# Kernel tuning notes

Measured on AMD Instinct MI355X. Metric: run time of the kernel, lower is better.

## Reference

```python
import jax, jax.numpy as jnp
import numpy as np

NEG = -9e15
ALPHA = 0.2  # leakyrelu slope


def setup_inputs() -> dict:
    key = jax.random.key(0)
    ks = jax.random.split(key, 12)
    bs, N, Fx, F, D = 8, 512, 8, 64, 16
    return {
        'input': jax.random.normal(ks[0], (bs, N, 1), jnp.float32),
        'adj': jax.random.randint(ks[1], (N, N), 0, 2, jnp.int32),
        'ext_input': jax.random.normal(ks[2], (bs, N, Fx), jnp.float32),
        'side_input': jax.random.normal(ks[3], (bs, N, 1), jnp.float32),
        'W': jax.random.normal(ks[4], (1, F), jnp.float32),
        'a': jax.random.normal(ks[5], (2 * F, 1), jnp.float32),
        'WS': jax.random.normal(ks[6], (1, F), jnp.float32),
        'aS': jax.random.normal(ks[7], (2 * F, 1), jnp.float32),
        'WQ': jax.random.normal(ks[8], (2, D), jnp.float32),
        'WK': jax.random.normal(ks[9], (2, D), jnp.float32),
        'WV': jax.random.normal(ks[10], (1, F), jnp.float32),
    }


def _pair_scores(h, a_vec):
    # e[b,i,j] = leakyrelu(a . [h_i, h_j]) ; equivalent to h@a1 + (h@a2)^T
    F = h.shape[-1]
    s1 = h @ a_vec[:F]          # [b,N,1]
    s2 = h @ a_vec[F:]          # [b,N,1]
    return jax.nn.leaky_relu(s1 + jnp.swapaxes(s2, 1, 2), negative_slope=ALPHA)


def reference(input, adj, ext_input, side_input, W, a, WS, aS, WQ, WK, WV):
    bs, N, _ = input.shape
    Fx = ext_input.shape[-1]
    D = WQ.shape[1]
    mask = (adj > 0)[None, :, :]  # [1,N,N] broadcasts over batch

    # ---- Step 1: node-channel GAT attention ----
    h = input @ W                    # [b,N,F]
    e = _pair_scores(h, a)           # [b,N,N]
    att = jnp.where(mask, e, NEG)
    h_side = side_input @ WS         # [b,N,F]
    e_side = _pair_scores(h_side, aS)
    att_side = jnp.where(mask, e_side, NEG)
    att = att + att_side
    att = jnp.where(att > 0, att, NEG)
    att = jax.nn.softmax(att, axis=2)             # [b,N,N]
    h_prime = jnp.einsum('bij,bjf->bif', att, h)  # [b,N,F]

    # ---- Step 2: ext-feature dot-product attention ----
    xs = input[..., 0]  # [b,N]
    # q[b,i,j,d] = (x_i*WQ[0,d] + x_j*WQ[1,d]) / sqrt(D)
    q = (xs[:, :, None, None] * WQ[0] + xs[:, None, :, None] * WQ[1]) / (D ** 0.5)
    # k[b,i,j,d,f] = ext_i_f*WK[0,d] + ext_j_f*WK[1,d]; dot = sum_d q*k, computed fused:
    qk0 = q @ WK[0]   # [b,N,N]
    qk1 = q @ WK[1]   # [b,N,N]
    dot = ext_input[:, :, None, :] * qk0[..., None] + ext_input[:, None, :, :] * qk1[..., None]  # [b,N,N,Fx]
    dot = jnp.where(dot > 0, dot, NEG)
    dot = jax.nn.softmax(dot, axis=3)
    final = dot * att[..., None]                 # [b,N,N,Fx]
    v = ext_input[..., None] * WV[0][None, None, None, :]  # [b,N,Fx,F]
    ext_rep = jnp.einsum('bijf,bife->bie', final, v)       # sum over j and f -> [b,N,F]

    return jax.nn.elu(h_prime), jax.nn.elu(ext_rep)
```

## Files before the change

kernel.cpp:

```cpp
#include <hip/hip_runtime.h>

#define NEGV (-9e15f)
#define LOG2E 1.44269504088896340736f

template<int CTRL>
__device__ __forceinline__ float dpp_add(float v) {
    const int t = __builtin_amdgcn_update_dpp(0, __float_as_int(v), CTRL, 0xf, 0xf, false);
    return v + __int_as_float(t);
}
template<int CTRL>
__device__ __forceinline__ float dpp_fmax(float v) {
    const int t = __builtin_amdgcn_update_dpp(__float_as_int(v), __float_as_int(v),
                                              CTRL, 0xf, 0xf, false);
    return fmaxf(v, __int_as_float(t));
}
__device__ __forceinline__ float rdlane(float v, int l) {
    return __int_as_float(__builtin_amdgcn_readlane(__float_as_int(v), l));
}
__device__ __forceinline__ float wsum(float v) {
    v = dpp_add<0x111>(v);
    v = dpp_add<0x112>(v);
    v = dpp_add<0x114>(v);
    v = dpp_add<0x118>(v);
    v = dpp_add<0x142>(v);
    v = dpp_add<0x143>(v);
    return rdlane(v, 63);
}
__device__ __forceinline__ float wmax(float v) {
    v = dpp_fmax<0x111>(v);
    v = dpp_fmax<0x112>(v);
    v = dpp_fmax<0x114>(v);
    v = dpp_fmax<0x118>(v);
    v = dpp_fmax<0x142>(v);
    v = dpp_fmax<0x143>(v);
    return rdlane(v, 63);
}
__device__ __forceinline__ float rowscan16(float v) {
    v = dpp_add<0x111>(v);
    v = dpp_add<0x112>(v);
    v = dpp_add<0x114>(v);
    v = dpp_add<0x118>(v);
    return v;
}
__device__ __forceinline__ void ld8f(const float* p, float* o) {
    const float4 v0 = ((const float4*)p)[0];
    const float4 v1 = ((const float4*)p)[1];
    o[0] = v0.x; o[1] = v0.y; o[2] = v0.z; o[3] = v0.w;
    o[4] = v1.x; o[5] = v1.y; o[6] = v1.z; o[7] = v1.w;
}

__global__ __launch_bounds__(64) void sentinel_kernel(float* __restrict__ out) {
    out[blockIdx.x * 64 + threadIdx.x] = 111222.0f;
}

__global__ __launch_bounds__(128, 4) void gat_fused_f32(
    const float* __restrict__ input, const int* __restrict__ adj,
    const float* __restrict__ ext, const float* __restrict__ side,
    const float* __restrict__ W, const float* __restrict__ a,
    const float* __restrict__ WS, const float* __restrict__ aS,
    const float* __restrict__ WQ, const float* __restrict__ WK,
    const float* __restrict__ WV, float* __restrict__ out)
{
    const int N = 512, F = 64;
    const int lane = threadIdx.x & 63;
    const int w = threadIdx.x >> 6;
    const int b = blockIdx.x >> 8;
    const int i0 = (blockIdx.x & 255) * 2;

    __shared__ float mrg[16];

    const int jbase = 256 * w;

    const float* ebase = ext + (size_t)(b * N + jbase) * 8;
    float4 stA[4], stB[4];
#pragma unroll
    for (int u = 0; u < 4; u++) {
        const float* p = ebase + (size_t)(u * 64 + lane) * 8;
        stA[u] = ((const float4*)p)[0];
        stB[u] = ((const float4*)p)[1];
    }

    const bool adj64 = (__any(adj[2 * lane + 1] != 0) == 0);

    const float wf  = W[lane];
    const float wvf = WV[lane];
    const float c1  = wsum(wf * a[lane]) * LOG2E;
    const float c2  = wsum(wf * a[F + lane]) * LOG2E;
    const float wsf = WS[lane];
    const float cS1 = wsum(wsf * aS[lane]) * LOG2E;
    const float cS2 = wsum(wsf * aS[F + lane]) * LOG2E;

    const int g = lane >> 4, l16 = lane & 15;
    const float QS = 0.25f * LOG2E;
    float prod = WQ[(g >> 1) * 16 + l16] * WK[(g & 1) * 16 + l16];
    prod = rowscan16(prod);
    const float a00 = rdlane(prod, 15) * QS;
    const float a01 = rdlane(prod, 31) * QS;
    const float a10 = rdlane(prod, 47) * QS;
    const float a11 = rdlane(prod, 63) * QS;

    const int row0 = b * N + i0;
    const float x0 = input[row0], x1 = input[row0 + 1];
    const float y0 = side[row0],  y1 = side[row0 + 1];
    float ei0[8], ei1[8];
    ld8f(ext + (size_t)row0 * 8, ei0);
    ld8f(ext + (size_t)(row0 + 1) * 8, ei1);

    const float s10 = c1 * x0,  s11 = c1 * x1;
    const float t10 = cS1 * y0, t11 = cS1 * y1;

    const float* xp = input + b * N + jbase;
    const float* yp = side + b * N + jbase;
    const int arow0 = i0 * N + jbase;
    const int* adji0 = adj + arow0;
    const int* adji1 = adji0 + N;
    const long long* adjl0 = (const long long*)adj + arow0;
    const long long* adjl1 = adjl0 + N;

    float xj[4], L0[4], L1[4];
#pragma unroll
    for (int t = 0; t < 4; t++) {
        const int jj = lane + 64 * t;
        const float xv = xp[jj];
        const float yv = yp[jj];
        xj[t] = xv;
        const float z  = c2 * xv;
        const float zs = cS2 * yv;
        float u0 = s10 + z;  u0 = fmaxf(u0, 0.2f * u0);
        float v0 = t10 + zs; v0 = fmaxf(v0, 0.2f * v0);
        float u1 = s11 + z;  u1 = fmaxf(u1, 0.2f * u1);
        float v1 = t11 + zs; v1 = fmaxf(v1, 0.2f * v1);
        const float g0 = u0 + v0;
        const float g1 = u1 + v1;
        int m0, m1;
        if (adj64) { m0 = (adjl0[jj] != 0); m1 = (adjl1[jj] != 0); }
        else       { m0 = adji0[jj];        m1 = adji1[jj]; }
        L0[t] = (m0 != 0 && g0 > 0.f) ? g0 : NEGV;
        L1[t] = (m1 != 0 && g1 > 0.f) ? g1 : NEGV;
    }
    float M0 = fmaxf(fmaxf(L0[0], L0[1]), fmaxf(L0[2], L0[3]));
    float M1 = fmaxf(fmaxf(L1[0], L1[1]), fmaxf(L1[2], L1[3]));
    M0 = wmax(M0); M1 = wmax(M1);

    float s0 = 0.f, s1 = 0.f;
#pragma unroll
    for (int t = 0; t < 4; t++) {
        L0[t] = __builtin_amdgcn_exp2f(L0[t] - M0); s0 += L0[t];
        L1[t] = __builtin_amdgcn_exp2f(L1[t] - M1); s1 += L1[t];
    }

    float A0 = 0.f, A1 = 0.f, R0 = 0.f, R1 = 0.f;
#pragma unroll
    for (int t = 0; t < 4; t++) {
        float ej[8];
        ej[0] = stA[t].x; ej[1] = stA[t].y; ej[2] = stA[t].z; ej[3] = stA[t].w;
        ej[4] = stB[t].x; ej[5] = stB[t].y; ej[6] = stB[t].z; ej[7] = stB[t].w;

        const float qj0 = xj[t] * a10, qj1 = xj[t] * a11;
        const float qk00 = x0 * a00 + qj0, qk01 = x0 * a01 + qj1;
        const float qk10 = x1 * a00 + qj0, qk11 = x1 * a01 + qj1;

        float d0[8], d1[8];
        float dm0 = NEGV, dm1 = NEGV;
#pragma unroll
        for (int f = 0; f < 8; f++) {
            float dv0 = ei0[f] * qk00 + ej[f] * qk01;
            float dv1 = ei1[f] * qk10 + ej[f] * qk11;
            dv0 = (dv0 > 0.f) ? dv0 : NEGV;
            dv1 = (dv1 > 0.f) ? dv1 : NEGV;
            d0[f] = dv0; dm0 = fmaxf(dm0, dv0);
            d1[f] = dv1; dm1 = fmaxf(dm1, dv1);
        }
        float ds0 = 0.f, ds1 = 0.f, dot0 = 0.f, dot1 = 0.f;
#pragma unroll
        for (int f = 0; f < 8; f++) {
            const float e0 = __builtin_amdgcn_exp2f(d0[f] - dm0);
            const float e1 = __builtin_amdgcn_exp2f(d1[f] - dm1);
            ds0 += e0; dot0 += e0 * ei0[f];
            ds1 += e1; dot1 += e1 * ei1[f];
        }
        A0 += L0[t] * xj[t];
        A1 += L1[t] * xj[t];
        R0 += L0[t] * __builtin_amdgcn_rcpf(ds0) * dot0;
        R1 += L1[t] * __builtin_amdgcn_rcpf(ds1) * dot1;
    }
    s0 = wsum(s0); s1 = wsum(s1);
    A0 = wsum(A0); A1 = wsum(A1);
    R0 = wsum(R0); R1 = wsum(R1);

    if (lane == 0) {
        float* m = mrg + w * 8;
        m[0] = M0; m[1] = M1; m[2] = s0; m[3] = s1;
        m[4] = A0; m[5] = A1; m[6] = R0; m[7] = R1;
    }
    __syncthreads();

    const float Ma0 = fmaxf(mrg[0], mrg[8]);
    const float Ma1 = fmaxf(mrg[1], mrg[9]);
    const float p00 = __builtin_amdgcn_exp2f(mrg[0] - Ma0);
    const float p01 = __builtin_amdgcn_exp2f(mrg[8] - Ma0);
    const float p10 = __builtin_amdgcn_exp2f(mrg[1] - Ma1);
    const float p11 = __builtin_amdgcn_exp2f(mrg[9] - Ma1);
    const float inv0 = __builtin_amdgcn_rcpf(p00 * mrg[2] + p01 * mrg[10]);
    const float inv1 = __builtin_amdgcn_rcpf(p10 * mrg[3] + p11 * mrg[11]);

    const int o = row0 * F + lane;
    if (w == 0) {
        float o00 = (p00 * mrg[4] + p01 * mrg[12]) * inv0 * wf;
        float o01 = (p10 * mrg[5] + p11 * mrg[13]) * inv1 * wf;
        o00 = (o00 > 0.f) ? o00 : (__builtin_amdgcn_exp2f(o00 * LOG2E) - 1.f);
        o01 = (o01 > 0.f) ? o01 : (__builtin_amdgcn_exp2f(o01 * LOG2E) - 1.f);
        out[o] = o00;
        out[o + F] = o01;
    } else {
        float o10 = (p00 * mrg[6] + p01 * mrg[14]) * inv0 * wvf;
        float o11 = (p10 * mrg[7] + p11 * mrg[15]) * inv1 * wvf;
        o10 = (o10 > 0.f) ? o10 : (__builtin_amdgcn_exp2f(o10 * LOG2E) - 1.f);
        o11 = (o11 > 0.f) ? o11 : (__builtin_amdgcn_exp2f(o11 * LOG2E) - 1.f);
        out[262144 + o] = o10;
        out[262144 + o + F] = o11;
    }
}

extern "C" void kernel_launch(void* const* d_in, const int* in_sizes, int n_in,
                              void* d_out, int out_size, void* d_ws, size_t ws_size,
                              hipStream_t stream) {
    static const int exp_sizes[11] = {4096, 262144, 32768, 4096, 64, 128, 64, 128, 32, 32, 64};
    bool ok = (n_in == 11) && (out_size == 524288);
    if (ok) {
        for (int k = 0; k < 11; k++) if (in_sizes[k] != exp_sizes[k]) ok = false;
    }
    if (!ok) {
        sentinel_kernel<<<4096, 64, 0, stream>>>((float*)d_out);
        return;
    }

    gat_fused_f32<<<2048, 128, 0, stream>>>(
        (const float*)d_in[0], (const int*)d_in[1],
        (const float*)d_in[2], (const float*)d_in[3],
        (const float*)d_in[4], (const float*)d_in[5],
        (const float*)d_in[6], (const float*)d_in[7],
        (const float*)d_in[8], (const float*)d_in[9],
        (const float*)d_in[10],
        (float*)d_out);
}
```

Before: 14.80 us.

## Hoist global loads early and drop max-subtraction in inner softmax

Issues the adjacency, input and side loads at kernel start so their latency overlaps the weight reductions, and loads adj as int by default, reloading as int64 only when the probe detects that layout. The per-pair 8-way softmax drops its max pass: positive logits are exponentiated directly with a clamp at 120, and the all-nonpositive case falls back to a uniform mean of ext. This removes one max loop and its temporaries, but numerics can differ from the max-shifted form when logits are near the clamp.

```diff
diff --git a/kernel.cpp b/kernel.cpp
--- a/kernel.cpp
+++ b/kernel.cpp
@@ -70,6 +70,25 @@
     __shared__ float mrg[16];
 
     const int jbase = 256 * w;
+    const int arow0 = i0 * N + jbase;
+    const int row0 = b * N + i0;
+
+    const int probe = adj[2 * lane + 1];
+
+    const int* adji0 = adj + arow0;
+    const int* adji1 = adji0 + N;
+    int m0i[4], m1i[4];
+    float xv[4], yv[4];
+    const float* xp = input + b * N + jbase;
+    const float* yp = side + b * N + jbase;
+#pragma unroll
+    for (int t = 0; t < 4; t++) {
+        const int jj = lane + 64 * t;
+        m0i[t] = adji0[jj];
+        m1i[t] = adji1[jj];
+        xv[t] = xp[jj];
+        yv[t] = yp[jj];
+    }
 
     const float* ebase = ext + (size_t)(b * N + jbase) * 8;
     float4 stA[4], stB[4];
@@ -80,63 +99,65 @@
         stB[u] = ((const float4*)p)[1];
     }
 
-    const bool adj64 = (__any(adj[2 * lane + 1] != 0) == 0);
-
-    const float wf  = W[lane];
-    const float wvf = WV[lane];
-    const float c1  = wsum(wf * a[lane]) * LOG2E;
-    const float c2  = wsum(wf * a[F + lane]) * LOG2E;
-    const float wsf = WS[lane];
-    const float cS1 = wsum(wsf * aS[lane]) * LOG2E;
-    const float cS2 = wsum(wsf * aS[F + lane]) * LOG2E;
-
-    const int g = lane >> 4, l16 = lane & 15;
-    const float QS = 0.25f * LOG2E;
-    float prod = WQ[(g >> 1) * 16 + l16] * WK[(g & 1) * 16 + l16];
-    prod = rowscan16(prod);
-    const float a00 = rdlane(prod, 15) * QS;
-    const float a01 = rdlane(prod, 31) * QS;
-    const float a10 = rdlane(prod, 47) * QS;
-    const float a11 = rdlane(prod, 63) * QS;
-
-    const int row0 = b * N + i0;
     const float x0 = input[row0], x1 = input[row0 + 1];
     const float y0 = side[row0],  y1 = side[row0 + 1];
     float ei0[8], ei1[8];
     ld8f(ext + (size_t)row0 * 8, ei0);
     ld8f(ext + (size_t)(row0 + 1) * 8, ei1);
 
+    const float wf  = W[lane];
+    const float wvf = WV[lane];
+    const float al1 = a[lane],  al2 = a[F + lane];
+    const float bl1 = aS[lane], bl2 = aS[F + lane];
+    const float wsf = WS[lane];
+    const int g = lane >> 4, l16 = lane & 15;
+    const float wq = WQ[(g >> 1) * 16 + l16];
+    const float wk = WK[(g & 1) * 16 + l16];
+
+    const bool adj64 = (__any(probe != 0) == 0);
+    if (adj64) {
+        const long long* adjl0 = (const long long*)adj + arow0;
+        const long long* adjl1 = adjl0 + N;
+#pragma unroll
+        for (int t = 0; t < 4; t++) {
+            const int jj = lane + 64 * t;
+            m0i[t] = (adjl0[jj] != 0);
+            m1i[t] = (adjl1[jj] != 0);
+        }
+    }
+
+    const float c1  = wsum(wf * al1) * LOG2E;
+    const float c2  = wsum(wf * al2) * LOG2E;
+    const float cS1 = wsum(wsf * bl1) * LOG2E;
+    const float cS2 = wsum(wsf * bl2) * LOG2E;
+    const float QS = 0.25f * LOG2E;
+    float prod = rowscan16(wq * wk);
+    const float a00 = rdlane(prod, 15) * QS;
+    const float a01 = rdlane(prod, 31) * QS;
+    const float a10 = rdlane(prod, 47) * QS;
+    const float a11 = rdlane(prod, 63) * QS;
+
     const float s10 = c1 * x0,  s11 = c1 * x1;
     const float t10 = cS1 * y0, t11 = cS1 * y1;
 
-    const float* xp = input + b * N + jbase;
-    const float* yp = side + b * N + jbase;
-    const int arow0 = i0 * N + jbase;
-    const int* adji0 = adj + arow0;
-    const int* adji1 = adji0 + N;
-    const long long* adjl0 = (const long long*)adj + arow0;
-    const long long* adjl1 = adjl0 + N;
-
-    float xj[4], L0[4], L1[4];
-#pragma unroll
-    for (int t = 0; t < 4; t++) {
-        const int jj = lane + 64 * t;
-        const float xv = xp[jj];
-        const float yv = yp[jj];
-        xj[t] = xv;
-        const float z  = c2 * xv;
-        const float zs = cS2 * yv;
+    float se0 = 0.f, se1 = 0.f;
+#pragma unroll
+    for (int f = 0; f < 8; f++) { se0 += ei0[f]; se1 += ei1[f]; }
+    se0 *= 0.125f; se1 *= 0.125f;
+
+    float L0[4], L1[4];
+#pragma unroll
+    for (int t = 0; t < 4; t++) {
+        const float z  = c2 * xv[t];
+        const float zs = cS2 * yv[t];
         float u0 = s10 + z;  u0 = fmaxf(u0, 0.2f * u0);
         float v0 = t10 + zs; v0 = fmaxf(v0, 0.2f * v0);
         float u1 = s11 + z;  u1 = fmaxf(u1, 0.2f * u1);
         float v1 = t11 + zs; v1 = fmaxf(v1, 0.2f * v1);
         const float g0 = u0 + v0;
         const float g1 = u1 + v1;
-        int m0, m1;
-        if (adj64) { m0 = (adjl0[jj] != 0); m1 = (adjl1[jj] != 0); }
-        else       { m0 = adji0[jj];        m1 = adji1[jj]; }
-        L0[t] = (m0 != 0 && g0 > 0.f) ? g0 : NEGV;
-        L1[t] = (m1 != 0 && g1 > 0.f) ? g1 : NEGV;
+        L0[t] = (m0i[t] != 0 && g0 > 0.f) ? g0 : NEGV;
+        L1[t] = (m1i[t] != 0 && g1 > 0.f) ? g1 : NEGV;
     }
     float M0 = fmaxf(fmaxf(L0[0], L0[1]), fmaxf(L0[2], L0[3]));
     float M1 = fmaxf(fmaxf(L1[0], L1[1]), fmaxf(L1[2], L1[3]));
@@ -156,31 +177,26 @@
         ej[0] = stA[t].x; ej[1] = stA[t].y; ej[2] = stA[t].z; ej[3] = stA[t].w;
         ej[4] = stB[t].x; ej[5] = stB[t].y; ej[6] = stB[t].z; ej[7] = stB[t].w;
 
-        const float qj0 = xj[t] * a10, qj1 = xj[t] * a11;
+        const float qj0 = xv[t] * a10, qj1 = xv[t] * a11;
         const float qk00 = x0 * a00 + qj0, qk01 = x0 * a01 + qj1;
         const float qk10 = x1 * a00 + qj0, qk11 = x1 * a01 + qj1;
 
-        float d0[8], d1[8];
-        float dm0 = NEGV, dm1 = NEGV;
+        float ds0 = 0.f, ds1 = 0.f, dot0 = 0.f, dot1 = 0.f;
 #pragma unroll
         for (int f = 0; f < 8; f++) {
-            float dv0 = ei0[f] * qk00 + ej[f] * qk01;
-            float dv1 = ei1[f] * qk10 + ej[f] * qk11;
-            dv0 = (dv0 > 0.f) ? dv0 : NEGV;
-            dv1 = (dv1 > 0.f) ? dv1 : NEGV;
-            d0[f] = dv0; dm0 = fmaxf(dm0, dv0);
-            d1[f] = dv1; dm1 = fmaxf(dm1, dv1);
-        }
-        float ds0 = 0.f, ds1 = 0.f, dot0 = 0.f, dot1 = 0.f;
-#pragma unroll
-        for (int f = 0; f < 8; f++) {
-            const float e0 = __builtin_amdgcn_exp2f(d0[f] - dm0);
-            const float e1 = __builtin_amdgcn_exp2f(d1[f] - dm1);
+            const float dv0 = ei0[f] * qk00 + ej[f] * qk01;
+            const float dv1 = ei1[f] * qk10 + ej[f] * qk11;
+            const float e0 = (dv0 > 0.f) ? __builtin_amdgcn_exp2f(fminf(dv0, 120.f)) : 0.f;
+            const float e1 = (dv1 > 0.f) ? __builtin_amdgcn_exp2f(fminf(dv1, 120.f)) : 0.f;
             ds0 += e0; dot0 += e0 * ei0[f];
             ds1 += e1; dot1 += e1 * ei1[f];
         }
-        A0 += L0[t] * xj[t];
-        A1 += L1[t] * xj[t];
+        const bool z0 = (ds0 == 0.f), z1 = (ds1 == 0.f);
+        dot0 = z0 ? se0 : dot0;  ds0 = z0 ? 1.f : ds0;
+        dot1 = z1 ? se1 : dot1;  ds1 = z1 ? 1.f : ds1;
+
+        A0 += L0[t] * xv[t];
+        A1 += L1[t] * xv[t];
         R0 += L0[t] * __builtin_amdgcn_rcpf(ds0) * dot0;
         R1 += L1[t] * __builtin_amdgcn_rcpf(ds1) * dot1;
     }
```

Result: slower. 19.89 us (+34.4%).
